# Optimization experiments

Measured on AMD Instinct MI355X. Metric: run time of the kernel, lower is better.

Reference implementation:

```python
import jax, jax.numpy as jnp
import numpy as np

N_DRUG = 8000
N_DIS = 8000
E = 524288  # edges per relation (avg degree 64)
N_REL = 4   # 0: drug->drug, 1: drug->disease, 2: disease->drug, 3: disease->disease


def setup_inputs() -> dict:
    key = jax.random.key(0)
    ks = jax.random.split(key, 11)
    inp = {
        "feat_drug": jax.random.normal(ks[0], (N_DRUG, N_DRUG), jnp.float32),
        "feat_dis": jax.random.normal(ks[1], (N_DIS, N_DIS), jnp.float32),
        "W_drug": jax.random.normal(ks[2], (N_DRUG, 64), jnp.float32) * 0.02,
        "W_dis": jax.random.normal(ks[3], (N_DIS, 64), jnp.float32) * 0.02,
        "W1": jax.random.normal(ks[4], (N_REL, 64, 64), jnp.float32) * 0.125,
        "b1": jnp.zeros((N_REL, 64), jnp.float32),
        "W2": jax.random.normal(ks[5], (N_REL, 64, 32), jnp.float32) * 0.15,
        "b2": jnp.zeros((N_REL, 32), jnp.float32),
        "Wf": jax.random.normal(ks[6], (32, 32), jnp.float32) * 0.25,
        "src": jax.random.randint(ks[7], (N_REL, E), 0, N_DRUG, jnp.int32),
        "dst": jax.random.randint(ks[8], (N_REL, E), 0, N_DIS, jnp.int32),
    }
    return inp


def _gconv(h_src, s, d, W, b, n_src, n_dst):
    # DGL GraphConv, norm='both': D_out^{-1/2} on src, sum-aggregate, D_in^{-1/2} on dst, + bias.
    ones = jnp.ones(s.shape, jnp.float32)
    deg_o = jnp.clip(jax.ops.segment_sum(ones, s, num_segments=n_src), 1.0)
    deg_i = jnp.clip(jax.ops.segment_sum(ones, d, num_segments=n_dst), 1.0)
    m = (h_src * jax.lax.rsqrt(deg_o)[:, None]) @ W      # [n_src, out]
    agg = jax.ops.segment_sum(m[s], d, num_segments=n_dst)  # gather-scatter SpMM
    return agg * jax.lax.rsqrt(deg_i)[:, None] + b


def _hetero_layer(h_drug, h_dis, src, dst, W, b):
    # HeteroGraphConv(aggregate='sum'): sum per-relation GraphConv outputs per dst type.
    new_drug = (_gconv(h_drug, src[0], dst[0], W[0], b[0], N_DRUG, N_DRUG)
                + _gconv(h_dis, src[2], dst[2], W[2], b[2], N_DIS, N_DRUG))
    new_dis = (_gconv(h_drug, src[1], dst[1], W[1], b[1], N_DRUG, N_DIS)
               + _gconv(h_dis, src[3], dst[3], W[3], b[3], N_DIS, N_DIS))
    return new_drug, new_dis


def reference(feat_drug, feat_dis, W_drug, W_dis, W1, b1, W2, b2, Wf, src, dst):
    # input embeddings (Linear, no bias)
    h_drug = feat_drug @ W_drug   # [N_DRUG, 64]
    h_dis = feat_dis @ W_dis      # [N_DIS, 64]
    # hetero layer 1 (64 -> 64) + ReLU (dropout is identity in eval)
    h_drug, h_dis = _hetero_layer(h_drug, h_dis, src, dst, W1, b1)
    h_drug, h_dis = jax.nn.relu(h_drug), jax.nn.relu(h_dis)
    # hetero layer 2 (64 -> 32) + ReLU
    h_drug, h_dis = _hetero_layer(h_drug, h_dis, src, dst, W2, b2)
    h_drug, h_dis = jax.nn.relu(h_drug), jax.nn.relu(h_dis)
    # bilinear scoring: (h_drug Wf^T) h_dis^T -> [N_DRUG, N_DIS]
    return (h_drug @ Wf.T) @ h_dis.T
```

## Files before the change

kernel.cpp:

```cpp
#include <hip/hip_runtime.h>
#include <hip/hip_bf16.h>

#define N_NODE 8000
#define EDGES  524288
#define LOG2E  19
#define NREL   4

__global__ void count_kernel(const int* __restrict__ src, const int* __restrict__ dst,
                             int* __restrict__ cnt_o, int* __restrict__ cnt_i) {
    int t = blockIdx.x * blockDim.x + threadIdx.x;
    if (t >= NREL * EDGES) return;
    int r = t >> LOG2E;
    atomicAdd(&cnt_o[r * N_NODE + src[t]], 1);
    atomicAdd(&cnt_i[r * N_NODE + dst[t]], 1);
}

__global__ void rdeg_kernel(const int* __restrict__ cnt, float* __restrict__ rdeg, int n) {
    int t = blockIdx.x * blockDim.x + threadIdx.x;
    if (t < n) rdeg[t] = rsqrtf((float)max(cnt[t], 1));
}

__global__ __launch_bounds__(1024) void scan_kernel(const int* __restrict__ cnt,
                                                    int* __restrict__ off, int* __restrict__ cursor) {
    __shared__ int buf[1024];
    __shared__ int sbase;
    if (threadIdx.x == 0) sbase = 0;
    __syncthreads();
    for (int c = 0; c < 32; ++c) {
        int i = c * 1024 + threadIdx.x;
        int v = (i < NREL * N_NODE) ? cnt[i] : 0;
        buf[threadIdx.x] = v;
        __syncthreads();
        for (int s = 1; s < 1024; s <<= 1) {
            int t = (threadIdx.x >= s) ? buf[threadIdx.x - s] : 0;
            __syncthreads();
            buf[threadIdx.x] += t;
            __syncthreads();
        }
        int b = sbase;
        if (i < NREL * N_NODE) {
            int excl = b + buf[threadIdx.x] - v;
            off[i] = excl;
            cursor[i] = excl;
        }
        __syncthreads();
        if (threadIdx.x == 1023) sbase = b + buf[1023];
        __syncthreads();
    }
}

__global__ void place_kernel(const int* __restrict__ src, const int* __restrict__ dst,
                             int* __restrict__ cursor, unsigned short* __restrict__ csr) {
    int t = blockIdx.x * blockDim.x + threadIdx.x;
    if (t >= NREL * EDGES) return;
    int r = t >> LOG2E;
    int pos = atomicAdd(&cursor[r * N_NODE + dst[t]], 1);
    csr[pos] = (unsigned short)src[t];
}

__global__ __launch_bounds__(256) void embed_gemm(
    const float* __restrict__ A, const float* __restrict__ W,
    float* __restrict__ C, int M, int K, int k_per_split) {
    __shared__ float sAT[32][132];
    __shared__ float sW[32][68];
    const int tid = threadIdx.x;
    const int tx = tid & 15, ty = tid >> 4;
    const int row0 = blockIdx.x * 128;
    const int kb = blockIdx.y * k_per_split;
    const int ke = kb + k_per_split;
    float acc[8][4] = {};

    for (int kk0 = kb; kk0 < ke; kk0 += 32) {
        #pragma unroll
        for (int i = 0; i < 4; ++i) {
            int f = tid + i * 256;
            int r = f >> 3, k4 = f & 7;
            int row = min(row0 + r, M - 1);
            const float4 v = *(const float4*)(A + (size_t)row * K + kk0 + k4 * 4);
            sAT[k4 * 4 + 0][r] = v.x; sAT[k4 * 4 + 1][r] = v.y;
            sAT[k4 * 4 + 2][r] = v.z; sAT[k4 * 4 + 3][r] = v.w;
        }
        #pragma unroll
        for (int i = 0; i < 2; ++i) {
            int f = tid + i * 256;
            int kr = f >> 4, c4 = f & 15;
            *(float4*)&sW[kr][c4 * 4] = *(const float4*)(W + (size_t)(kk0 + kr) * 64 + c4 * 4);
        }
        __syncthreads();
        #pragma unroll
        for (int kk = 0; kk < 32; ++kk) {
            float4 a0 = *(const float4*)&sAT[kk][ty * 8];
            float4 a1 = *(const float4*)&sAT[kk][ty * 8 + 4];
            float4 w  = *(const float4*)&sW[kk][tx * 4];
            float av[8] = {a0.x, a0.y, a0.z, a0.w, a1.x, a1.y, a1.z, a1.w};
            float wv[4] = {w.x, w.y, w.z, w.w};
            #pragma unroll
            for (int i = 0; i < 8; ++i) {
                #pragma unroll
                for (int j = 0; j < 4; ++j)
                    acc[i][j] = fmaf(av[i], wv[j], acc[i][j]);
            }
        }
        __syncthreads();
    }
    #pragma unroll
    for (int i = 0; i < 8; ++i) {
        int row = row0 + ty * 8 + i;
        if (row < M) {
            #pragma unroll
            for (int j = 0; j < 4; ++j)
                atomicAdd(&C[(size_t)row * 64 + tx * 4 + j], acc[i][j]);
        }
    }
}

template<int K, int N>
__global__ __launch_bounds__(256) void gemm_small(
    const float* __restrict__ Adrug, const float* __restrict__ Adis,
    const float* __restrict__ Wall, const float* __restrict__ scaleAll,
    float* __restrict__ outAll, int M) {
    const int r = blockIdx.y;
    const float* A = (r < 2) ? Adrug : Adis;
    const float* W = Wall + (size_t)r * K * N;
    const float* scale = scaleAll ? (scaleAll + (size_t)r * N_NODE) : nullptr;
    float* O = outAll + (size_t)r * M * N;

    __shared__ float sAT[K][68];
    __shared__ float sW[K][N + 4];
    const int tid = threadIdx.x;
    const int tx = tid & 15, ty = tid >> 4;
    const int row0 = blockIdx.x * 64;
    constexpr int NC = N / 16;

    constexpr int AF4 = 64 * K / 4 / 256;
    #pragma unroll
    for (int i = 0; i < AF4; ++i) {
        int f = tid + i * 256;
        int rr = f / (K / 4), k4 = f % (K / 4);
        int row = row0 + rr;
        float s = scale ? scale[row] : 1.0f;
        const float4 v = *(const float4*)(A + (size_t)row * K + k4 * 4);
        sAT[k4 * 4 + 0][rr] = v.x * s; sAT[k4 * 4 + 1][rr] = v.y * s;
        sAT[k4 * 4 + 2][rr] = v.z * s; sAT[k4 * 4 + 3][rr] = v.w * s;
    }
    constexpr int WF4 = K * N / 4 / 256;
    #pragma unroll
    for (int i = 0; i < WF4; ++i) {
        int f = tid + i * 256;
        int kr = f / (N / 4), c4 = f % (N / 4);
        *(float4*)&sW[kr][c4 * 4] = *(const float4*)(W + (size_t)kr * N + c4 * 4);
    }
    __syncthreads();

    float acc[4][NC] = {};
    #pragma unroll
    for (int kk = 0; kk < K; ++kk) {
        float4 a = *(const float4*)&sAT[kk][ty * 4];
        float av[4] = {a.x, a.y, a.z, a.w};
        float wv[NC];
        if constexpr (NC == 4) {
            float4 w = *(const float4*)&sW[kk][tx * 4];
            wv[0] = w.x; wv[1] = w.y; wv[2] = w.z; wv[3] = w.w;
        } else {
            float2 w = *(const float2*)&sW[kk][tx * 2];
            wv[0] = w.x; wv[1] = w.y;
        }
        #pragma unroll
        for (int i = 0; i < 4; ++i) {
            #pragma unroll
            for (int j = 0; j < NC; ++j)
                acc[i][j] = fmaf(av[i], wv[j], acc[i][j]);
        }
    }
    #pragma unroll
    for (int i = 0; i < 4; ++i) {
        int row = row0 + ty * 4 + i;
        if constexpr (NC == 4) {
            float4 v = {acc[i][0], acc[i][1], acc[i][2], acc[i][3]};
            *(float4*)(O + (size_t)row * N + tx * 4) = v;
        } else {
            float2 v = {acc[i][0], acc[i][1]};
            *(float2*)(O + (size_t)row * N + tx * 2) = v;
        }
    }
}

template<int N>
__global__ __launch_bounds__(256) void gather_combine(
    const float* __restrict__ m, const unsigned short* __restrict__ csr,
    const int* __restrict__ off, const int* __restrict__ cnt,
    const float* __restrict__ rdeg_i, const float* __restrict__ bias,
    float* __restrict__ outDrug, float* __restrict__ outDis) {
    constexpr int NPW = 64 / N;
    const int lane = threadIdx.x & 63;
    const int wave = threadIdx.x >> 6;
    const int sub = lane / N;
    const int f = lane % N;
    const int node = (blockIdx.x * 4 + wave) * NPW + sub;
    if (node >= N_NODE) return;
    const int typ = blockIdx.y;
    const int ra = (typ == 0) ? 0 : 1, rb = (typ == 0) ? 2 : 3;

    float acc[2] = {0.0f, 0.0f};
    const int rels[2] = {ra, rb};
    #pragma unroll
    for (int q = 0; q < 2; ++q) {
        const int rid = rels[q] * N_NODE + node;
        const int beg = off[rid];
        const int c = cnt[rid];
        const float* mr = m + (size_t)rels[q] * N_NODE * N;
        int k = 0;
        for (; k + 4 <= c; k += 4) {
            int s0 = csr[beg + k], s1 = csr[beg + k + 1];
            int s2 = csr[beg + k + 2], s3 = csr[beg + k + 3];
            float v0 = mr[s0 * N + f], v1 = mr[s1 * N + f];
            float v2 = mr[s2 * N + f], v3 = mr[s3 * N + f];
            acc[q] += (v0 + v1) + (v2 + v3);
        }
        for (; k < c; ++k) acc[q] += mr[csr[beg + k] * N + f];
    }
    float o = acc[0] * rdeg_i[ra * N_NODE + node] + acc[1] * rdeg_i[rb * N_NODE + node]
            + bias[ra * N + f] + bias[rb * N + f];
    o = fmaxf(o, 0.0f);
    (typ == 0 ? outDrug : outDis)[(size_t)node * N + f] = o;
}

__global__ __launch_bounds__(256) void gemm_nt_final(
    const float* __restrict__ A, const float* __restrict__ B,
    float* __restrict__ C, int M, int Nc) {
    __shared__ float sAT[32][132];
    __shared__ float sBT[32][68];
    const int tid = threadIdx.x;
    const int tx = tid & 15, ty = tid >> 4;
    const int row0 = blockIdx.x * 128, col0 = blockIdx.y * 64;
    #pragma unroll
    for (int i = 0; i < 4; ++i) {
        int f = tid + i * 256;
        int r = f >> 3, k4 = f & 7;
        int row = min(row0 + r, M - 1);
        const float4 v = *(const float4*)(A + (size_t)row * 32 + k4 * 4);
        sAT[k4 * 4 + 0][r] = v.x; sAT[k4 * 4 + 1][r] = v.y;
        sAT[k4 * 4 + 2][r] = v.z; sAT[k4 * 4 + 3][r] = v.w;
    }
    #pragma unroll
    for (int i = 0; i < 2; ++i) {
        int f = tid + i * 256;
        int br = f >> 3, k4 = f & 7;
        const float4 v = *(const float4*)(B + (size_t)(col0 + br) * 32 + k4 * 4);
        sBT[k4 * 4 + 0][br] = v.x; sBT[k4 * 4 + 1][br] = v.y;
        sBT[k4 * 4 + 2][br] = v.z; sBT[k4 * 4 + 3][br] = v.w;
    }
    __syncthreads();
    float acc[8][4] = {};
    #pragma unroll
    for (int a = 0; a < 32; ++a) {
        float4 a0 = *(const float4*)&sAT[a][ty * 8];
        float4 a1 = *(const float4*)&sAT[a][ty * 8 + 4];
        float4 b4 = *(const float4*)&sBT[a][tx * 4];
        float av[8] = {a0.x, a0.y, a0.z, a0.w, a1.x, a1.y, a1.z, a1.w};
        float bv[4] = {b4.x, b4.y, b4.z, b4.w};
        #pragma unroll
        for (int i = 0; i < 8; ++i) {
            #pragma unroll
            for (int j = 0; j < 4; ++j)
                acc[i][j] = fmaf(av[i], bv[j], acc[i][j]);
        }
    }
    #pragma unroll
    for (int i = 0; i < 8; ++i) {
        int row = row0 + ty * 8 + i;
        if (row < M) {
            float4 v = {acc[i][0], acc[i][1], acc[i][2], acc[i][3]};
            *(float4*)(C + (size_t)row * Nc + col0 + tx * 4) = v;
        }
    }
}

extern "C" void kernel_launch(void* const* d_in, const int* in_sizes, int n_in,
                              void* d_out, int out_size, void* d_ws, size_t ws_size,
                              hipStream_t stream) {
    const float* feat_drug = (const float*)d_in[0];
    const float* feat_dis  = (const float*)d_in[1];
    const float* W_drug    = (const float*)d_in[2];
    const float* W_dis     = (const float*)d_in[3];
    const float* W1        = (const float*)d_in[4];
    const float* b1        = (const float*)d_in[5];
    const float* W2        = (const float*)d_in[6];
    const float* b2        = (const float*)d_in[7];
    const float* Wf        = (const float*)d_in[8];
    const int*   src       = (const int*)d_in[9];
    const int*   dst       = (const int*)d_in[10];
    float* out = (float*)d_out;

    float* fbase   = (float*)d_ws;
    float* rdeg_o  = fbase;
    float* rdeg_i  = fbase + 32000;
    float* h_drug  = fbase + 64000;
    float* h_dis   = fbase + 576000;
    float* m       = fbase + 1088000;
    float* h2_drug = fbase + 3136000;
    float* h2_dis  = fbase + 3392000;
    float* g       = fbase + 3648000;
    int*   ibase   = (int*)(fbase + 3904000);
    int*   cnt_o   = ibase;
    int*   cnt_i   = ibase + 32000;
    int*   off     = ibase + 64000;
    int*   cursor  = ibase + 96000;
    unsigned short* csr = (unsigned short*)(ibase + 128000);
    float* h1_drug = h_drug;
    float* h1_dis  = h_dis;

    hipMemsetAsync(cnt_o, 0, 64000 * sizeof(int), stream);
    hipMemsetAsync(h_drug, 0, 1024000 * sizeof(float), stream);

    count_kernel<<<8192, 256, 0, stream>>>(src, dst, cnt_o, cnt_i);
    rdeg_kernel<<<125, 256, 0, stream>>>(cnt_o, rdeg_o, 32000);
    rdeg_kernel<<<125, 256, 0, stream>>>(cnt_i, rdeg_i, 32000);
    scan_kernel<<<1, 1024, 0, stream>>>(cnt_i, off, cursor);
    place_kernel<<<8192, 256, 0, stream>>>(src, dst, cursor, csr);

    dim3 ge(63, 25);
    embed_gemm<<<ge, 256, 0, stream>>>(feat_drug, W_drug, h_drug, N_NODE, N_NODE, 320);
    embed_gemm<<<ge, 256, 0, stream>>>(feat_dis,  W_dis,  h_dis,  N_NODE, N_NODE, 320);

    gemm_small<64, 64><<<dim3(125, 4), 256, 0, stream>>>(h_drug, h_dis, W1, rdeg_o, m, N_NODE);
    gather_combine<64><<<dim3(2000, 2), 256, 0, stream>>>(m, csr, off, cnt_i, rdeg_i, b1, h1_drug, h1_dis);

    gemm_small<64, 32><<<dim3(125, 4), 256, 0, stream>>>(h1_drug, h1_dis, W2, rdeg_o, m, N_NODE);
    gather_combine<32><<<dim3(1000, 2), 256, 0, stream>>>(m, csr, off, cnt_i, rdeg_i, b2, h2_drug, h2_dis);

    gemm_small<32, 32><<<dim3(125, 1), 256, 0, stream>>>(h2_dis, h2_dis, Wf, nullptr, g, N_NODE);
    gemm_nt_final<<<dim3(63, 125), 256, 0, stream>>>(h2_drug, g, out, N_NODE, N_NODE);
}
```

Before: 1.385 ms.

## Restructure embed GEMM with register prefetch, 64-row tiles and fewer K splits

```diff
diff --git a/kernel.cpp b/kernel.cpp
--- a/kernel.cpp
+++ b/kernel.cpp
@@ -60,57 +60,75 @@
 
 __global__ __launch_bounds__(256) void embed_gemm(
     const float* __restrict__ A, const float* __restrict__ W,
-    float* __restrict__ C, int M, int K, int k_per_split) {
-    __shared__ float sAT[32][132];
+    float* __restrict__ C, int K, int k_per_split) {
+    __shared__ float sA[64][36];
     __shared__ float sW[32][68];
     const int tid = threadIdx.x;
     const int tx = tid & 15, ty = tid >> 4;
-    const int row0 = blockIdx.x * 128;
+    const int row0 = blockIdx.x * 64;
     const int kb = blockIdx.y * k_per_split;
-    const int ke = kb + k_per_split;
-    float acc[8][4] = {};
-
-    for (int kk0 = kb; kk0 < ke; kk0 += 32) {
+    const int nt = k_per_split / 32;
+
+    const int ar = tid >> 3, ak4 = tid & 7;
+    const int wk = tid >> 4, wc4 = tid & 15;
+    const float* Ap0 = A + (size_t)(row0 + ar) * K + ak4 * 4;
+    const float* Ap1 = A + (size_t)(row0 + ar + 32) * K + ak4 * 4;
+    const float* Wp0 = W + (size_t)wk * 64 + wc4 * 4;
+    const float* Wp1 = W + (size_t)(wk + 16) * 64 + wc4 * 4;
+
+    float4 pa0, pa1, pw0, pw1;
+    pa0 = *(const float4*)(Ap0 + kb);
+    pa1 = *(const float4*)(Ap1 + kb);
+    pw0 = *(const float4*)(Wp0 + (size_t)kb * 64);
+    pw1 = *(const float4*)(Wp1 + (size_t)kb * 64);
+
+    float acc[4][4] = {};
+
+    for (int t = 0; t < nt; ++t) {
+        *(float4*)&sA[ar][ak4 * 4] = pa0;
+        *(float4*)&sA[ar + 32][ak4 * 4] = pa1;
+        *(float4*)&sW[wk][wc4 * 4] = pw0;
+        *(float4*)&sW[wk + 16][wc4 * 4] = pw1;
+        __syncthreads();
+        if (t + 1 < nt) {
+            int kk0 = kb + (t + 1) * 32;
+            pa0 = *(const float4*)(Ap0 + kk0);
+            pa1 = *(const float4*)(Ap1 + kk0);
+            pw0 = *(const float4*)(Wp0 + (size_t)kk0 * 64);
+            pw1 = *(const float4*)(Wp1 + (size_t)kk0 * 64);
+        }
         #pragma unroll
-        for (int i = 0; i < 4; ++i) {
-            int f = tid + i * 256;
-            int r = f >> 3, k4 = f & 7;
-            int row = min(row0 + r, M - 1);
-            const float4 v = *(const float4*)(A + (size_t)row * K + kk0 + k4 * 4);
-            sAT[k4 * 4 + 0][r] = v.x; sAT[k4 * 4 + 1][r] = v.y;
-            sAT[k4 * 4 + 2][r] = v.z; sAT[k4 * 4 + 3][r] = v.w;
-        }
+        for (int q = 0; q < 8; ++q) {
+            float4 a0 = *(const float4*)&sA[ty * 4 + 0][q * 4];
+            float4 a1 = *(const float4*)&sA[ty * 4 + 1][q * 4];
+            float4 a2 = *(const float4*)&sA[ty * 4 + 2][q * 4];
+            float4 a3 = *(const float4*)&sA[ty * 4 + 3][q * 4];
+            float4 w0 = *(const float4*)&sW[q * 4 + 0][tx * 4];
+            float4 w1 = *(const float4*)&sW[q * 4 + 1][tx * 4];
+            float4 w2 = *(const float4*)&sW[q * 4 + 2][tx * 4];
+            float4 w3 = *(const float4*)&sW[q * 4 + 3][tx * 4];
+            float av[4][4] = {{a0.x, a0.y, a0.z, a0.w}, {a1.x, a1.y, a1.z, a1.w},
+                              {a2.x, a2.y, a2.z, a2.w}, {a3.x, a3.y, a3.z, a3.w}};
+            float wv[4][4] = {{w0.x, w0.y, w0.z, w0.w}, {w1.x, w1.y, w1.z, w1.w},
+                              {w2.x, w2.y, w2.z, w2.w}, {w3.x, w3.y, w3.z, w3.w}};
+            #pragma unroll
+            for (int i = 0; i < 4; ++i) {
+                #pragma unroll
+                for (int j = 0; j < 4; ++j) {
+                    #pragma unroll
+                    for (int kk = 0; kk < 4; ++kk)
+                        acc[i][j] = fmaf(av[i][kk], wv[kk][j], acc[i][j]);
+                }
+            }
+        }
+        __syncthreads();
+    }
+    #pragma unroll
+    for (int i = 0; i < 4; ++i) {
+        float* cp = &C[(size_t)(row0 + ty * 4 + i) * 64 + tx * 4];
         #pragma unroll
-        for (int i = 0; i < 2; ++i) {
-            int f = tid + i * 256;
-            int kr = f >> 4, c4 = f & 15;
-            *(float4*)&sW[kr][c4 * 4] = *(const float4*)(W + (size_t)(kk0 + kr) * 64 + c4 * 4);
-        }
-        __syncthreads();
-        #pragma unroll
-        for (int kk = 0; kk < 32; ++kk) {
-            float4 a0 = *(const float4*)&sAT[kk][ty * 8];
-            float4 a1 = *(const float4*)&sAT[kk][ty * 8 + 4];
-            float4 w  = *(const float4*)&sW[kk][tx * 4];
-            float av[8] = {a0.x, a0.y, a0.z, a0.w, a1.x, a1.y, a1.z, a1.w};
-            float wv[4] = {w.x, w.y, w.z, w.w};
-            #pragma unroll
-            for (int i = 0; i < 8; ++i) {
-                #pragma unroll
-                for (int j = 0; j < 4; ++j)
-                    acc[i][j] = fmaf(av[i], wv[j], acc[i][j]);
-            }
-        }
-        __syncthreads();
-    }
-    #pragma unroll
-    for (int i = 0; i < 8; ++i) {
-        int row = row0 + ty * 8 + i;
-        if (row < M) {
-            #pragma unroll
-            for (int j = 0; j < 4; ++j)
-                atomicAdd(&C[(size_t)row * 64 + tx * 4 + j], acc[i][j]);
-        }
+        for (int j = 0; j < 4; ++j)
+            atomicAdd(cp + j, acc[i][j]);
     }
 }
 
@@ -319,9 +337,9 @@
     scan_kernel<<<1, 1024, 0, stream>>>(cnt_i, off, cursor);
     place_kernel<<<8192, 256, 0, stream>>>(src, dst, cursor, csr);
 
-    dim3 ge(63, 25);
-    embed_gemm<<<ge, 256, 0, stream>>>(feat_drug, W_drug, h_drug, N_NODE, N_NODE, 320);
-    embed_gemm<<<ge, 256, 0, stream>>>(feat_dis,  W_dis,  h_dis,  N_NODE, N_NODE, 320);
+    dim3 ge(125, 5);
+    embed_gemm<<<ge, 256, 0, stream>>>(feat_drug, W_drug, h_drug, N_NODE, 1600);
+    embed_gemm<<<ge, 256, 0, stream>>>(feat_dis,  W_dis,  h_dis,  N_NODE, 1600);
 
     gemm_small<64, 64><<<dim3(125, 4), 256, 0, stream>>>(h_drug, h_dis, W1, rdeg_o, m, N_NODE);
     gather_combine<64><<<dim3(2000, 2), 256, 0, stream>>>(m, csr, off, cnt_i, rdeg_i, b1, h1_drug, h1_dis);
```

Result: faster. 1.253 ms (-9.5%).
